# Performance work log

Hardware: AMD Instinct MI355X
Metric: run time of the kernel (lower is better)

## Reference

```python
import jax, jax.numpy as jnp
import numpy as np


def setup_inputs() -> dict:
    key = jax.random.key(0)
    k1, k2 = jax.random.split(key)
    N_KV, MAX_CTX, HEAD_DIM, CHUNK = 8, 32768, 128, 2048
    k_cache = jnp.zeros((1, N_KV, MAX_CTX, HEAD_DIM), dtype=jnp.float32)
    v_cache = jnp.zeros((1, N_KV, MAX_CTX, HEAD_DIM), dtype=jnp.float32)
    pos_ids = jnp.arange(CHUNK, dtype=jnp.int64)
    k = jax.random.normal(k1, (1, N_KV, CHUNK, HEAD_DIM), dtype=jnp.float32)
    v = jax.random.normal(k2, (1, N_KV, CHUNK, HEAD_DIM), dtype=jnp.float32)
    return {"k_cache": k_cache, "v_cache": v_cache, "pos_ids": pos_ids, "k": k, "v": v}


def reference(k_cache, v_cache, pos_ids, k, v):
    # kout[:, :, pos_ids, :] = k  (scatter write along the context axis)
    kout = k_cache.at[:, :, pos_ids, :].set(k)
    vout = v_cache.at[:, :, pos_ids, :].set(v)
    return (kout, vout)
```

## Files before the change

### kernel.cpp

```cpp
#include <hip/hip_runtime.h>


constexpr long N_KV     = 8;
constexpr long MAX_CTX  = 32768;
constexpr long HEAD_DIM = 128;
constexpr long CHUNK    = 2048;

constexpr long CACHE_ELEMS = N_KV * MAX_CTX * HEAD_DIM;
constexpr long CACHE_N4    = CACHE_ELEMS / 4;
constexpr long KV_ELEMS    = N_KV * CHUNK * HEAD_DIM;
constexpr long KV_N4       = KV_ELEMS / 4;
constexpr long C4          = HEAD_DIM / 4;

__global__ void kv_copy_kernel(const float4* __restrict__ kc,
                               const float4* __restrict__ vc,
                               float4* __restrict__ out_k,
                               float4* __restrict__ out_v) {
    long i      = (long)blockIdx.x * blockDim.x + threadIdx.x;
    long stride = (long)gridDim.x * blockDim.x;
    for (; i < CACHE_N4; i += stride) {
        out_k[i] = kc[i];
        out_v[i] = vc[i];
    }
}

__global__ void kv_scatter_kernel(const float4* __restrict__ k,
                                  const float4* __restrict__ v,
                                  const int* __restrict__ pos,
                                  float4* __restrict__ out_k,
                                  float4* __restrict__ out_v) {
    long i      = (long)blockIdx.x * blockDim.x + threadIdx.x;
    long stride = (long)gridDim.x * blockDim.x;
    for (; i < KV_N4; i += stride) {
        long col = i & (C4 - 1);
        long r   = i / C4;
        long row = r & (CHUNK - 1);
        long h   = r / CHUNK;
        long p   = (long)pos[row];
        long o   = (h * MAX_CTX + p) * C4 + col;
        out_k[o] = k[i];
        out_v[o] = v[i];
    }
}

extern "C" void kernel_launch(void* const* d_in, const int* in_sizes, int n_in,
                              void* d_out, int out_size, void* d_ws, size_t ws_size,
                              hipStream_t stream) {
    const float4* k_cache = (const float4*)d_in[0];
    const float4* v_cache = (const float4*)d_in[1];
    const int*    pos     = (const int*)  d_in[2];
    const float4* k       = (const float4*)d_in[3];
    const float4* v       = (const float4*)d_in[4];

    float* out   = (float*)d_out;
    float4* out_k = (float4*)out;
    float4* out_v = (float4*)(out + CACHE_ELEMS);

    {
        int block = 256;
        long want = (CACHE_N4 + block - 1) / block;
        int grid  = (int)(want > 32768 ? 32768 : want);
        kv_copy_kernel<<<grid, block, 0, stream>>>(k_cache, v_cache, out_k, out_v);
    }
    {
        int block = 256;
        int grid  = (int)((KV_N4 + block - 1) / block);
        kv_scatter_kernel<<<grid, block, 0, stream>>>(k, v, pos, out_k, out_v);
    }
}
```

Baseline: 447.8 us.

## Fuse cache copy and scatter via inverse position map with nontemporal accesses

```diff
diff --git a/kernel.cpp b/kernel.cpp
--- a/kernel.cpp
+++ b/kernel.cpp
@@ -1,70 +1,77 @@
 #include <hip/hip_runtime.h>
 
 
-constexpr long N_KV     = 8;
-constexpr long MAX_CTX  = 32768;
-constexpr long HEAD_DIM = 128;
-constexpr long CHUNK    = 2048;
+typedef float v4f __attribute__((ext_vector_type(4)));
 
-constexpr long CACHE_ELEMS = N_KV * MAX_CTX * HEAD_DIM;
+constexpr int  N_KV     = 8;
+constexpr int  MAX_CTX  = 32768;
+constexpr int  HEAD_DIM = 128;
+constexpr int  CHUNK    = 2048;
+
+constexpr long CACHE_ELEMS = (long)N_KV * MAX_CTX * HEAD_DIM;
 constexpr long CACHE_N4    = CACHE_ELEMS / 4;
-constexpr long KV_ELEMS    = N_KV * CHUNK * HEAD_DIM;
-constexpr long KV_N4       = KV_ELEMS / 4;
-constexpr long C4          = HEAD_DIM / 4;
+constexpr int  C4          = HEAD_DIM / 4;
 
-__global__ void kv_copy_kernel(const float4* __restrict__ kc,
-                               const float4* __restrict__ vc,
-                               float4* __restrict__ out_k,
-                               float4* __restrict__ out_v) {
-    long i      = (long)blockIdx.x * blockDim.x + threadIdx.x;
-    long stride = (long)gridDim.x * blockDim.x;
-    for (; i < CACHE_N4; i += stride) {
-        out_k[i] = kc[i];
-        out_v[i] = vc[i];
-    }
+__global__ void inv_init_kernel(int* __restrict__ inv) {
+    int i = blockIdx.x * blockDim.x + threadIdx.x;
+    if (i < MAX_CTX) inv[i] = -1;
 }
 
-__global__ void kv_scatter_kernel(const float4* __restrict__ k,
-                                  const float4* __restrict__ v,
-                                  const int* __restrict__ pos,
-                                  float4* __restrict__ out_k,
-                                  float4* __restrict__ out_v) {
-    long i      = (long)blockIdx.x * blockDim.x + threadIdx.x;
-    long stride = (long)gridDim.x * blockDim.x;
-    for (; i < KV_N4; i += stride) {
-        long col = i & (C4 - 1);
-        long r   = i / C4;
-        long row = r & (CHUNK - 1);
-        long h   = r / CHUNK;
-        long p   = (long)pos[row];
-        long o   = (h * MAX_CTX + p) * C4 + col;
-        out_k[o] = k[i];
-        out_v[o] = v[i];
+__global__ void inv_fill_kernel(const int* __restrict__ pos, int* __restrict__ inv) {
+    int j = blockIdx.x * blockDim.x + threadIdx.x;
+    if (j < CHUNK) inv[pos[j]] = j;
+}
+
+__global__ void kv_fused_kernel(const v4f* __restrict__ kc,
+                                const v4f* __restrict__ vc,
+                                const v4f* __restrict__ k,
+                                const v4f* __restrict__ v,
+                                const int* __restrict__ inv,
+                                v4f* __restrict__ out_k,
+                                v4f* __restrict__ out_v) {
+    long i = (long)blockIdx.x * blockDim.x + threadIdx.x;
+    if (i >= CACHE_N4) return;
+    int  col = (int)(i & (C4 - 1));
+    long r   = i >> 5;
+    int  row = (int)(r & (MAX_CTX - 1));
+    int  h   = (int)(r >> 15);
+    int  j   = inv[row];
+
+    v4f a, b;
+    if (j >= 0) {
+        long s = ((long)h * CHUNK + j) * C4 + col;
+        a = k[s];
+        b = v[s];
+    } else {
+        a = __builtin_nontemporal_load(&kc[i]);
+        b = __builtin_nontemporal_load(&vc[i]);
     }
+    __builtin_nontemporal_store(a, &out_k[i]);
+    __builtin_nontemporal_store(b, &out_v[i]);
 }
 
 extern "C" void kernel_launch(void* const* d_in, const int* in_sizes, int n_in,
                               void* d_out, int out_size, void* d_ws, size_t ws_size,
                               hipStream_t stream) {
-    const float4* k_cache = (const float4*)d_in[0];
-    const float4* v_cache = (const float4*)d_in[1];
-    const int*    pos     = (const int*)  d_in[2];
-    const float4* k       = (const float4*)d_in[3];
-    const float4* v       = (const float4*)d_in[4];
+    const v4f* k_cache = (const v4f*)d_in[0];
+    const v4f* v_cache = (const v4f*)d_in[1];
+    const int* pos     = (const int*)d_in[2];
+    const v4f* k       = (const v4f*)d_in[3];
+    const v4f* v       = (const v4f*)d_in[4];
 
     float* out   = (float*)d_out;
-    float4* out_k = (float4*)out;
-    float4* out_v = (float4*)(out + CACHE_ELEMS);
+    v4f*   out_k = (v4f*)out;
+    v4f*   out_v = (v4f*)(out + CACHE_ELEMS);
+
+    int* inv = (int*)d_ws;
+
+    inv_init_kernel<<<MAX_CTX / 256, 256, 0, stream>>>(inv);
+    inv_fill_kernel<<<CHUNK / 256, 256, 0, stream>>>(pos, inv);
 
     {
-        int block = 256;
-        long want = (CACHE_N4 + block - 1) / block;
-        int grid  = (int)(want > 32768 ? 32768 : want);
-        kv_copy_kernel<<<grid, block, 0, stream>>>(k_cache, v_cache, out_k, out_v);
-    }
-    {
-        int block = 256;
-        int grid  = (int)((KV_N4 + block - 1) / block);
-        kv_scatter_kernel<<<grid, block, 0, stream>>>(k, v, pos, out_k, out_v);
+        int  block = 256;
+        long grid  = (CACHE_N4 + block - 1) / block;
+        kv_fused_kernel<<<(int)grid, block, 0, stream>>>(k_cache, v_cache, k, v,
+                                                         inv, out_k, out_v);
     }
 }
```

After: 456.8 us. +2.0%, slower.
